# Optimization experiments

Hardware: AMD Instinct MI355X
Metric: run time of the kernel (lower is better)

Reference implementation:

```python
import jax, jax.numpy as jnp
import numpy as np

N_NODES = 50000
N_EDGES = 800000
IN_FEAT = 64
OUT_FEAT = 64
NUM_RELS = 200


def setup_inputs() -> dict:
    key = jax.random.key(0)
    ks = jax.random.split(key, 7)
    feat = jax.random.normal(ks[0], (N_NODES, IN_FEAT), dtype=jnp.float32)
    rel = jax.random.normal(ks[1], (NUM_RELS, IN_FEAT), dtype=jnp.float32)
    # xavier_uniform with relu gain ~ sqrt(2)*sqrt(6/(fan_in+fan_out))
    lim_wn = np.sqrt(2.0) * np.sqrt(6.0 / (4 * IN_FEAT + OUT_FEAT))
    weight_neighbor = jax.random.uniform(ks[2], (4 * IN_FEAT, OUT_FEAT), minval=-lim_wn, maxval=lim_wn, dtype=jnp.float32)
    lim_lw = np.sqrt(2.0) * np.sqrt(6.0 / (IN_FEAT + OUT_FEAT))
    loop_weight = jax.random.uniform(ks[3], (IN_FEAT, OUT_FEAT), minval=-lim_lw, maxval=lim_lw, dtype=jnp.float32)
    src = jax.random.randint(ks[4], (N_EDGES,), 0, N_NODES, dtype=jnp.int32)
    dst = jax.random.randint(ks[5], (N_EDGES,), 0, N_NODES, dtype=jnp.int32)
    etype = jax.random.randint(ks[6], (N_EDGES,), 0, NUM_RELS, dtype=jnp.int32)
    return {"feat": feat, "rel": rel, "weight_neighbor": weight_neighbor,
            "loop_weight": loop_weight, "src": src, "dst": dst, "etype": etype}


def reference(feat, rel, weight_neighbor, loop_weight, src, dst, etype):
    n = feat.shape[0]
    # edge gather
    h = feat[src]            # [E, F]
    r = rel[etype]           # [E, F]
    # message: concat([h+r, h*r, h, r]) @ W  -> [E, out]
    m = jnp.concatenate([h + r, h * r, h, r], axis=1) @ weight_neighbor
    # mean scatter-reduce to destination nodes (zero for isolated nodes, like DGL)
    s = jax.ops.segment_sum(m, dst, num_segments=n)
    cnt = jax.ops.segment_sum(jnp.ones((dst.shape[0],), feat.dtype), dst, num_segments=n)
    agg = s / jnp.maximum(cnt, 1.0)[:, None]
    # self loop (activation=None, dropout=0.0 -> identity)
    return agg + feat @ loop_weight
```

## Files before the change

### kernel.cpp

```cpp
#include <hip/hip_runtime.h>

#define F 64
#define CAP 64
#define CAPB 4608
#define EPB 2048
#define XSTR 264

typedef __attribute__((ext_vector_type(8))) short bf16x8;
typedef __attribute__((ext_vector_type(4))) float f32x4;

__device__ __forceinline__ unsigned short f2b(float x) {
    unsigned int u = __float_as_uint(x);
    return (unsigned short)((u + 0x7FFFu + ((u >> 16) & 1u)) >> 16);
}

__global__ void k_pre(const float* __restrict__ wn, const float* __restrict__ lw,
                      unsigned short* __restrict__ wcb, int* __restrict__ bin_cursor,
                      int nbin) {
    int i = blockIdx.x * 256 + threadIdx.x;
    if (i < nbin) bin_cursor[i] = 0;
    int lane = (i >> 3) & 63, j = i & 7;
    int kt = i >> 11, nt = (i >> 9) & 3;
    int k = kt * 32 + ((lane >> 4) << 3) + j;
    int n = nt * 16 + (lane & 15);
    float v;
    if (k < 64)
        v = wn[k * 64 + n] + wn[(128 + k) * 64 + n];
    else if (k < 128)
        v = wn[(k - 64) * 64 + n] + wn[(k + 128) * 64 + n];
    else if (k < 192)
        v = wn[(k - 64) * 64 + n];
    else
        v = lw[(k - 192) * 64 + n];
    wcb[i] = f2b(v);
}

__global__ __launch_bounds__(256) void k_bin(
    const int* __restrict__ src, const int* __restrict__ dst,
    const int* __restrict__ et, int* __restrict__ bin_cursor,
    unsigned int* __restrict__ coarse, int e) {
    __shared__ int hist[256];
    __shared__ int cur[256];

    const int t = threadIdx.x;
    hist[t] = 0;
    __syncthreads();

    const int i0 = blockIdx.x * EPB + t * 8;
    int s[8], d[8], r[8];
    int nv = 0;
    if (i0 + 8 <= e) {
        int4 sa = ((const int4*)(src + i0))[0], sb = ((const int4*)(src + i0))[1];
        int4 da = ((const int4*)(dst + i0))[0], db = ((const int4*)(dst + i0))[1];
        int4 ta = ((const int4*)(et  + i0))[0], tb = ((const int4*)(et  + i0))[1];
        s[0]=sa.x; s[1]=sa.y; s[2]=sa.z; s[3]=sa.w; s[4]=sb.x; s[5]=sb.y; s[6]=sb.z; s[7]=sb.w;
        d[0]=da.x; d[1]=da.y; d[2]=da.z; d[3]=da.w; d[4]=db.x; d[5]=db.y; d[6]=db.z; d[7]=db.w;
        r[0]=ta.x; r[1]=ta.y; r[2]=ta.z; r[3]=ta.w; r[4]=tb.x; r[5]=tb.y; r[6]=tb.z; r[7]=tb.w;
        nv = 8;
    } else {
        for (int q = 0; q < 8; ++q) {
            int i = i0 + q;
            if (i < e) { s[q] = src[i]; d[q] = dst[i]; r[q] = et[i]; nv = q + 1; }
        }
    }

    for (int q = 0; q < nv; ++q) atomicAdd(&hist[d[q] >> 8], 1);
    __syncthreads();

    if (hist[t] > 0) cur[t] = atomicAdd(&bin_cursor[t], hist[t]);
    __syncthreads();

    for (int q = 0; q < nv; ++q) {
        int b = d[q] >> 8;
        int pos = atomicAdd(&cur[b], 1);
        if (pos < CAPB)
            coarse[b * CAPB + pos] = (unsigned int)s[q] | ((unsigned int)r[q] << 16)
                                   | ((unsigned int)(d[q] & 255) << 24);
    }
}

__global__ __launch_bounds__(1024) void k_build(
    const unsigned int* __restrict__ coarse, const int* __restrict__ bin_cursor,
    unsigned int* __restrict__ bucket, int* __restrict__ cnt, int n) {
    __shared__ int lcnt[256];
    const int t = threadIdx.x, b = blockIdx.x;
    if (t < 256) lcnt[t] = 0;
    __syncthreads();
    int ne = bin_cursor[b]; if (ne > CAPB) ne = CAPB;
    for (int i = t; i < ne; i += 1024) {
        unsigned int u = coarse[b * CAPB + i];
        int dl = (int)(u >> 24);
        int rk = atomicAdd(&lcnt[dl], 1);
        if (rk < CAP) bucket[(((b << 8) | dl) * CAP) + rk] = u & 0xFFFFFFu;
    }
    __syncthreads();
    int node = (b << 8) + t;
    if (t < 256 && node < n) cnt[node] = lcnt[t];
}

#define NPW 4

__global__ __launch_bounds__(256, 8) void k_main(
    const float* __restrict__ feat, const float* __restrict__ rel,
    const unsigned short* __restrict__ wcb, const int* __restrict__ cnt,
    const unsigned int* __restrict__ bucket,
    float* __restrict__ out, int n_nodes) {

    __shared__ unsigned short xb[16 * XSTR];

    const int lane = threadIdx.x & 63;
    const int wid  = threadIdx.x >> 6;
    const int node0 = (blockIdx.x * 4 + wid) * NPW;

#pragma unroll
    for (int n = 0; n < NPW; ++n) {
        int v = node0 + n;
        float sH = 0.f, sR = 0.f, sHR = 0.f, f0 = 0.f;
        if (v < n_nodes) {
            int deg = cnt[v];
            int m = deg < CAP ? deg : CAP;
            unsigned int pk = (lane < m) ? bucket[v * CAP + lane] : 0u;
            int j = 0;
            for (; j + 8 <= m; j += 8) {
                float h[8], r[8];
#pragma unroll
                for (int q = 0; q < 8; ++q) {
                    int u = __builtin_amdgcn_readlane((int)pk, j + q);
                    h[q] = feat[((u & 0xFFFF) << 6) + lane];
                    r[q] = rel[(((u >> 16) & 0xFF) << 6) + lane];
                }
#pragma unroll
                for (int q = 0; q < 8; ++q) {
                    sH += h[q]; sR += r[q]; sHR += h[q] * r[q];
                }
            }
            for (; j < m; ++j) {
                int u = __builtin_amdgcn_readlane((int)pk, j);
                float h = feat[((u & 0xFFFF) << 6) + lane];
                float r = rel[(((u >> 16) & 0xFF) << 6) + lane];
                sH += h; sR += r; sHR += h * r;
            }
            float inv = (deg > 0) ? 1.0f / (float)deg : 1.0f;
            sH *= inv; sR *= inv; sHR *= inv;
            f0 = feat[v * F + lane];
        }
        unsigned short* X = &xb[(wid * NPW + n) * XSTR];
        X[lane]       = f2b(sH);
        X[64 + lane]  = f2b(sR);
        X[128 + lane] = f2b(sHR);
        X[192 + lane] = f2b(f0);
    }
    __syncthreads();

    f32x4 acc = {0.f, 0.f, 0.f, 0.f};
    const int am = lane & 15, aq = lane >> 4;
#pragma unroll
    for (int kt = 0; kt < 8; ++kt) {
        bf16x8 a = *(const bf16x8*)&xb[am * XSTR + kt * 32 + aq * 8];
        bf16x8 b = *(const bf16x8*)&wcb[(((kt * 4 + wid) * 64) + lane) * 8];
        acc = __builtin_amdgcn_mfma_f32_16x16x32_bf16(a, b, acc, 0, 0, 0);
    }

    const int colbase = wid * 16 + am;
#pragma unroll
    for (int reg = 0; reg < 4; ++reg) {
        int v = blockIdx.x * 16 + aq * 4 + reg;
        if (v < n_nodes) out[v * F + colbase] = acc[reg];
    }
}

extern "C" void kernel_launch(void* const* d_in, const int* in_sizes, int n_in,
                              void* d_out, int out_size, void* d_ws, size_t ws_size,
                              hipStream_t stream) {
    const float* feat = (const float*)d_in[0];
    const float* rel  = (const float*)d_in[1];
    const float* wn   = (const float*)d_in[2];
    const float* lw   = (const float*)d_in[3];
    const int* src = (const int*)d_in[4];
    const int* dst = (const int*)d_in[5];
    const int* et  = (const int*)d_in[6];
    float* out = (float*)d_out;

    const int N = in_sizes[0] / F;
    const int E = in_sizes[4];
    const int nbin = (N + 255) >> 8;

    int* ws = (int*)d_ws;
    int* bin_cursor      = ws;
    int* cnt             = ws + 256;
    unsigned int* coarse = (unsigned int*)(cnt + N);
    unsigned int* bucket = coarse + (size_t)nbin * CAPB;
    unsigned short* wcb  = (unsigned short*)(bucket + (size_t)N * CAP);

    k_pre<<<64, 256, 0, stream>>>(wn, lw, wcb, bin_cursor, nbin);
    k_bin<<<(E + EPB - 1) / EPB, 256, 0, stream>>>(src, dst, et, bin_cursor, coarse, E);
    k_build<<<nbin, 1024, 0, stream>>>(coarse, bin_cursor, bucket, cnt, N);
    int blocks = (N + 15) / 16;
    k_main<<<blocks, 256, 0, stream>>>(feat, rel, wcb, cnt, bucket, out, N);
}
```

Before: 137.6 us.

## Gather two edges per wave with float2 half-wave loads; enlarge binning blocks

The main gather loop now has each half-wave fetch a different edge's 64-float row as float2 loads, so one wave instruction covers two edges. The two halves' partial sums are combined with a cross-half shuffle before the bf16 packing, and the LDS stores become packed 32-bit writes split between halves. Separately, the binning kernel processes twice as many edges per block with 512 threads, which halves the number of blocks and global cursor atomics. The aim is fewer load instructions and more bytes per load in the gather, at the cost of extra shuffles and select logic for odd-degree tails.

```diff
diff --git a/kernel.cpp b/kernel.cpp
--- a/kernel.cpp
+++ b/kernel.cpp
@@ -3,7 +3,7 @@
 #define F 64
 #define CAP 64
 #define CAPB 4608
-#define EPB 2048
+#define EPB 4096
 #define XSTR 264
 
 typedef __attribute__((ext_vector_type(8))) short bf16x8;
@@ -35,7 +35,7 @@
     wcb[i] = f2b(v);
 }
 
-__global__ __launch_bounds__(256) void k_bin(
+__global__ __launch_bounds__(512) void k_bin(
     const int* __restrict__ src, const int* __restrict__ dst,
     const int* __restrict__ et, int* __restrict__ bin_cursor,
     unsigned int* __restrict__ coarse, int e) {
@@ -43,7 +43,7 @@
     __shared__ int cur[256];
 
     const int t = threadIdx.x;
-    hist[t] = 0;
+    if (t < 256) hist[t] = 0;
     __syncthreads();
 
     const int i0 = blockIdx.x * EPB + t * 8;
@@ -67,7 +67,7 @@
     for (int q = 0; q < nv; ++q) atomicAdd(&hist[d[q] >> 8], 1);
     __syncthreads();
 
-    if (hist[t] > 0) cur[t] = atomicAdd(&bin_cursor[t], hist[t]);
+    if (t < 256 && hist[t] > 0) cur[t] = atomicAdd(&bin_cursor[t], hist[t]);
     __syncthreads();
 
     for (int q = 0; q < nv; ++q) {
@@ -110,45 +110,74 @@
 
     const int lane = threadIdx.x & 63;
     const int wid  = threadIdx.x >> 6;
+    const int lf   = lane & 31;
+    const bool hi  = lane >= 32;
+    const float zm = hi ? 0.f : 1.f;
     const int node0 = (blockIdx.x * 4 + wid) * NPW;
+
+    const float2* f2 = (const float2*)feat;
+    const float2* r2 = (const float2*)rel;
 
 #pragma unroll
     for (int n = 0; n < NPW; ++n) {
         int v = node0 + n;
-        float sH = 0.f, sR = 0.f, sHR = 0.f, f0 = 0.f;
+        float2 sH = {0.f, 0.f}, sR = {0.f, 0.f}, sHR = {0.f, 0.f}, f02 = {0.f, 0.f};
         if (v < n_nodes) {
             int deg = cnt[v];
             int m = deg < CAP ? deg : CAP;
             unsigned int pk = (lane < m) ? bucket[v * CAP + lane] : 0u;
             int j = 0;
             for (; j + 8 <= m; j += 8) {
-                float h[8], r[8];
-#pragma unroll
-                for (int q = 0; q < 8; ++q) {
-                    int u = __builtin_amdgcn_readlane((int)pk, j + q);
-                    h[q] = feat[((u & 0xFFFF) << 6) + lane];
-                    r[q] = rel[(((u >> 16) & 0xFF) << 6) + lane];
+                float2 h[4], r[4];
+#pragma unroll
+                for (int p = 0; p < 4; ++p) {
+                    int u0 = __builtin_amdgcn_readlane((int)pk, j + 2 * p);
+                    int u1 = __builtin_amdgcn_readlane((int)pk, j + 2 * p + 1);
+                    int u = hi ? u1 : u0;
+                    h[p] = f2[((u & 0xFFFF) << 5) + lf];
+                    r[p] = r2[(((u >> 16) & 0xFF) << 5) + lf];
                 }
 #pragma unroll
-                for (int q = 0; q < 8; ++q) {
-                    sH += h[q]; sR += r[q]; sHR += h[q] * r[q];
+                for (int p = 0; p < 4; ++p) {
+                    sH.x += h[p].x;            sH.y += h[p].y;
+                    sR.x += r[p].x;            sR.y += r[p].y;
+                    sHR.x += h[p].x * r[p].x;  sHR.y += h[p].y * r[p].y;
                 }
             }
-            for (; j < m; ++j) {
+            for (; j + 2 <= m; j += 2) {
+                int u0 = __builtin_amdgcn_readlane((int)pk, j);
+                int u1 = __builtin_amdgcn_readlane((int)pk, j + 1);
+                int u = hi ? u1 : u0;
+                float2 h = f2[((u & 0xFFFF) << 5) + lf];
+                float2 r = r2[(((u >> 16) & 0xFF) << 5) + lf];
+                sH.x += h.x;          sH.y += h.y;
+                sR.x += r.x;          sR.y += r.y;
+                sHR.x += h.x * r.x;   sHR.y += h.y * r.y;
+            }
+            if (j < m) {
                 int u = __builtin_amdgcn_readlane((int)pk, j);
-                float h = feat[((u & 0xFFFF) << 6) + lane];
-                float r = rel[(((u >> 16) & 0xFF) << 6) + lane];
-                sH += h; sR += r; sHR += h * r;
+                float2 h = f2[((u & 0xFFFF) << 5) + lf];
+                float2 r = r2[(((u >> 16) & 0xFF) << 5) + lf];
+                h.x *= zm; h.y *= zm; r.x *= zm; r.y *= zm;
+                sH.x += h.x;          sH.y += h.y;
+                sR.x += r.x;          sR.y += r.y;
+                sHR.x += h.x * r.x;   sHR.y += h.y * r.y;
             }
+            sH.x += __shfl_xor(sH.x, 32);   sH.y += __shfl_xor(sH.y, 32);
+            sR.x += __shfl_xor(sR.x, 32);   sR.y += __shfl_xor(sR.y, 32);
+            sHR.x += __shfl_xor(sHR.x, 32); sHR.y += __shfl_xor(sHR.y, 32);
             float inv = (deg > 0) ? 1.0f / (float)deg : 1.0f;
-            sH *= inv; sR *= inv; sHR *= inv;
-            f0 = feat[v * F + lane];
+            sH.x *= inv; sH.y *= inv; sR.x *= inv; sR.y *= inv;
+            sHR.x *= inv; sHR.y *= inv;
+            f02 = f2[(v << 5) + lf];
         }
-        unsigned short* X = &xb[(wid * NPW + n) * XSTR];
-        X[lane]       = f2b(sH);
-        X[64 + lane]  = f2b(sR);
-        X[128 + lane] = f2b(sHR);
-        X[192 + lane] = f2b(f0);
+        unsigned int pH = ((unsigned int)f2b(sH.y) << 16) | f2b(sH.x);
+        unsigned int pR = ((unsigned int)f2b(sR.y) << 16) | f2b(sR.x);
+        unsigned int pQ = ((unsigned int)f2b(sHR.y) << 16) | f2b(sHR.x);
+        unsigned int pF = ((unsigned int)f2b(f02.y) << 16) | f2b(f02.x);
+        unsigned int* X32 = (unsigned int*)&xb[(wid * NPW + n) * XSTR];
+        if (!hi) { X32[lf] = pH;      X32[64 + lf] = pQ; }
+        else     { X32[32 + lf] = pR; X32[96 + lf] = pF; }
     }
     __syncthreads();
 
@@ -193,7 +222,7 @@
     unsigned short* wcb  = (unsigned short*)(bucket + (size_t)N * CAP);
 
     k_pre<<<64, 256, 0, stream>>>(wn, lw, wcb, bin_cursor, nbin);
-    k_bin<<<(E + EPB - 1) / EPB, 256, 0, stream>>>(src, dst, et, bin_cursor, coarse, E);
+    k_bin<<<(E + EPB - 1) / EPB, 512, 0, stream>>>(src, dst, et, bin_cursor, coarse, E);
     k_build<<<nbin, 1024, 0, stream>>>(coarse, bin_cursor, bucket, cnt, N);
     int blocks = (N + 15) / 16;
     k_main<<<blocks, 256, 0, stream>>>(feat, rel, wcb, cnt, bucket, out, N);
```

Result: no change. 135.2 us (-1.7%).

## Interleave two nodes' edge gathers per wave and widen binning blocks

Applied to the files above, without the earlier changes.

The main kernel now processes node pairs, issuing the 8-edge feature and relation gathers for both nodes before accumulating either. This puts more independent global loads in flight per wave to hide gather latency. The binning kernel moves to 1024-thread blocks handling 8192 edges each, which cuts global cursor atomics but launches far fewer blocks. Mean normalization now divides by the capped degree instead of the true degree, which only matters for nodes with more than 64 edges.

```diff
diff --git a/kernel.cpp b/kernel.cpp
--- a/kernel.cpp
+++ b/kernel.cpp
@@ -3,7 +3,7 @@
 #define F 64
 #define CAP 64
 #define CAPB 4608
-#define EPB 2048
+#define EPB 8192
 #define XSTR 264
 
 typedef __attribute__((ext_vector_type(8))) short bf16x8;
@@ -35,7 +35,7 @@
     wcb[i] = f2b(v);
 }
 
-__global__ __launch_bounds__(256) void k_bin(
+__global__ __launch_bounds__(1024) void k_bin(
     const int* __restrict__ src, const int* __restrict__ dst,
     const int* __restrict__ et, int* __restrict__ bin_cursor,
     unsigned int* __restrict__ coarse, int e) {
@@ -43,7 +43,7 @@
     __shared__ int cur[256];
 
     const int t = threadIdx.x;
-    hist[t] = 0;
+    if (t < 256) hist[t] = 0;
     __syncthreads();
 
     const int i0 = blockIdx.x * EPB + t * 8;
@@ -67,7 +67,7 @@
     for (int q = 0; q < nv; ++q) atomicAdd(&hist[d[q] >> 8], 1);
     __syncthreads();
 
-    if (hist[t] > 0) cur[t] = atomicAdd(&bin_cursor[t], hist[t]);
+    if (t < 256 && hist[t] > 0) cur[t] = atomicAdd(&bin_cursor[t], hist[t]);
     __syncthreads();
 
     for (int q = 0; q < nv; ++q) {
@@ -113,42 +113,78 @@
     const int node0 = (blockIdx.x * 4 + wid) * NPW;
 
 #pragma unroll
-    for (int n = 0; n < NPW; ++n) {
-        int v = node0 + n;
-        float sH = 0.f, sR = 0.f, sHR = 0.f, f0 = 0.f;
-        if (v < n_nodes) {
-            int deg = cnt[v];
-            int m = deg < CAP ? deg : CAP;
-            unsigned int pk = (lane < m) ? bucket[v * CAP + lane] : 0u;
-            int j = 0;
-            for (; j + 8 <= m; j += 8) {
-                float h[8], r[8];
-#pragma unroll
-                for (int q = 0; q < 8; ++q) {
-                    int u = __builtin_amdgcn_readlane((int)pk, j + q);
-                    h[q] = feat[((u & 0xFFFF) << 6) + lane];
-                    r[q] = rel[(((u >> 16) & 0xFF) << 6) + lane];
-                }
-#pragma unroll
-                for (int q = 0; q < 8; ++q) {
-                    sH += h[q]; sR += r[q]; sHR += h[q] * r[q];
-                }
-            }
-            for (; j < m; ++j) {
-                int u = __builtin_amdgcn_readlane((int)pk, j);
-                float h = feat[((u & 0xFFFF) << 6) + lane];
-                float r = rel[(((u >> 16) & 0xFF) << 6) + lane];
-                sH += h; sR += r; sHR += h * r;
-            }
-            float inv = (deg > 0) ? 1.0f / (float)deg : 1.0f;
-            sH *= inv; sR *= inv; sHR *= inv;
-            f0 = feat[v * F + lane];
-        }
-        unsigned short* X = &xb[(wid * NPW + n) * XSTR];
-        X[lane]       = f2b(sH);
-        X[64 + lane]  = f2b(sR);
-        X[128 + lane] = f2b(sHR);
-        X[192 + lane] = f2b(f0);
+    for (int np = 0; np < NPW; np += 2) {
+        const int va = node0 + np, vb = node0 + np + 1;
+        const int ma = (va < n_nodes) ? min(cnt[va], CAP) : 0;
+        const int mb = (vb < n_nodes) ? min(cnt[vb], CAP) : 0;
+        unsigned int pka = (lane < ma) ? bucket[va * CAP + lane] : 0u;
+        unsigned int pkb = (lane < mb) ? bucket[vb * CAP + lane] : 0u;
+        float sHa = 0.f, sRa = 0.f, sQa = 0.f;
+        float sHb = 0.f, sRb = 0.f, sQb = 0.f;
+        int ja = 0, jb = 0;
+
+        while ((ja + 8 <= ma) | (jb + 8 <= mb)) {
+            const bool da = (ja + 8 <= ma), db = (jb + 8 <= mb);
+            float ha[8], ra[8], hb[8], rb[8];
+            if (da) {
+#pragma unroll
+                for (int q = 0; q < 8; ++q) {
+                    int u = __builtin_amdgcn_readlane((int)pka, ja + q);
+                    ha[q] = feat[((u & 0xFFFF) << 6) + lane];
+                    ra[q] = rel[(((u >> 16) & 0xFF) << 6) + lane];
+                }
+            }
+            if (db) {
+#pragma unroll
+                for (int q = 0; q < 8; ++q) {
+                    int u = __builtin_amdgcn_readlane((int)pkb, jb + q);
+                    hb[q] = feat[((u & 0xFFFF) << 6) + lane];
+                    rb[q] = rel[(((u >> 16) & 0xFF) << 6) + lane];
+                }
+            }
+            if (da) {
+#pragma unroll
+                for (int q = 0; q < 8; ++q) {
+                    sHa += ha[q]; sRa += ra[q]; sQa += ha[q] * ra[q];
+                }
+                ja += 8;
+            }
+            if (db) {
+#pragma unroll
+                for (int q = 0; q < 8; ++q) {
+                    sHb += hb[q]; sRb += rb[q]; sQb += hb[q] * rb[q];
+                }
+                jb += 8;
+            }
+        }
+        for (; ja < ma; ++ja) {
+            int u = __builtin_amdgcn_readlane((int)pka, ja);
+            float h = feat[((u & 0xFFFF) << 6) + lane];
+            float r = rel[(((u >> 16) & 0xFF) << 6) + lane];
+            sHa += h; sRa += r; sQa += h * r;
+        }
+        for (; jb < mb; ++jb) {
+            int u = __builtin_amdgcn_readlane((int)pkb, jb);
+            float h = feat[((u & 0xFFFF) << 6) + lane];
+            float r = rel[(((u >> 16) & 0xFF) << 6) + lane];
+            sHb += h; sRb += r; sQb += h * r;
+        }
+
+        const float inva = (ma > 0) ? 1.0f / (float)ma : 1.0f;
+        const float invb = (mb > 0) ? 1.0f / (float)mb : 1.0f;
+        const float f0a = (va < n_nodes) ? feat[va * F + lane] : 0.f;
+        const float f0b = (vb < n_nodes) ? feat[vb * F + lane] : 0.f;
+
+        unsigned short* Xa = &xb[(wid * NPW + np) * XSTR];
+        Xa[lane]       = f2b(sHa * inva);
+        Xa[64 + lane]  = f2b(sRa * inva);
+        Xa[128 + lane] = f2b(sQa * inva);
+        Xa[192 + lane] = f2b(f0a);
+        unsigned short* Xb = &xb[(wid * NPW + np + 1) * XSTR];
+        Xb[lane]       = f2b(sHb * invb);
+        Xb[64 + lane]  = f2b(sRb * invb);
+        Xb[128 + lane] = f2b(sQb * invb);
+        Xb[192 + lane] = f2b(f0b);
     }
     __syncthreads();
 
@@ -193,7 +229,7 @@
     unsigned short* wcb  = (unsigned short*)(bucket + (size_t)N * CAP);
 
     k_pre<<<64, 256, 0, stream>>>(wn, lw, wcb, bin_cursor, nbin);
-    k_bin<<<(E + EPB - 1) / EPB, 256, 0, stream>>>(src, dst, et, bin_cursor, coarse, E);
+    k_bin<<<(E + EPB - 1) / EPB, 1024, 0, stream>>>(src, dst, et, bin_cursor, coarse, E);
     k_build<<<nbin, 1024, 0, stream>>>(coarse, bin_cursor, bucket, cnt, N);
     int blocks = (N + 15) / 16;
     k_main<<<blocks, 256, 0, stream>>>(feat, rel, wcb, cnt, bucket, out, N);
```

Result: no change. 135.1 us (-1.8%).

## Pre-convert feat and rel to bf16 for gathers; enlarge binning blocks

Applied to the files above, without the earlier changes.

Adds a conversion pass in the prologue kernel that writes bf16 copies of feat and rel, and the main kernel gathers from those copies, halving the bytes moved per random edge gather. The binning kernel also moves to 1024-thread blocks handling 8192 edges each, which cuts the number of blocks and the global cursor atomics. The conversion adds a full read and write of feat, and summing bf16-rounded inputs adds precision loss beyond the existing bf16 MFMA stage.

```diff
diff --git a/kernel.cpp b/kernel.cpp
--- a/kernel.cpp
+++ b/kernel.cpp
@@ -3,7 +3,7 @@
 #define F 64
 #define CAP 64
 #define CAPB 4608
-#define EPB 2048
+#define EPB 8192
 #define XSTR 264
 
 typedef __attribute__((ext_vector_type(8))) short bf16x8;
@@ -13,29 +13,50 @@
     unsigned int u = __float_as_uint(x);
     return (unsigned short)((u + 0x7FFFu + ((u >> 16) & 1u)) >> 16);
 }
+__device__ __forceinline__ float b2f(unsigned short b) {
+    return __uint_as_float(((unsigned int)b) << 16);
+}
 
 __global__ void k_pre(const float* __restrict__ wn, const float* __restrict__ lw,
-                      unsigned short* __restrict__ wcb, int* __restrict__ bin_cursor,
-                      int nbin) {
-    int i = blockIdx.x * 256 + threadIdx.x;
-    if (i < nbin) bin_cursor[i] = 0;
-    int lane = (i >> 3) & 63, j = i & 7;
-    int kt = i >> 11, nt = (i >> 9) & 3;
-    int k = kt * 32 + ((lane >> 4) << 3) + j;
-    int n = nt * 16 + (lane & 15);
-    float v;
-    if (k < 64)
-        v = wn[k * 64 + n] + wn[(128 + k) * 64 + n];
-    else if (k < 128)
-        v = wn[(k - 64) * 64 + n] + wn[(k + 128) * 64 + n];
-    else if (k < 192)
-        v = wn[(k - 64) * 64 + n];
-    else
-        v = lw[(k - 192) * 64 + n];
-    wcb[i] = f2b(v);
-}
-
-__global__ __launch_bounds__(256) void k_bin(
+                      const float* __restrict__ feat, const float* __restrict__ rel,
+                      unsigned short* __restrict__ wcb, unsigned short* __restrict__ fb,
+                      unsigned short* __restrict__ rb, int* __restrict__ bin_cursor,
+                      int nbin, int nf4, int nr4) {
+    if (blockIdx.x < 64) {
+        int i = blockIdx.x * 256 + threadIdx.x;
+        if (i < nbin) bin_cursor[i] = 0;
+        int lane = (i >> 3) & 63, j = i & 7;
+        int kt = i >> 11, nt = (i >> 9) & 3;
+        int k = kt * 32 + ((lane >> 4) << 3) + j;
+        int n = nt * 16 + (lane & 15);
+        float v;
+        if (k < 64)
+            v = wn[k * 64 + n] + wn[(128 + k) * 64 + n];
+        else if (k < 128)
+            v = wn[(k - 64) * 64 + n] + wn[(k + 128) * 64 + n];
+        else if (k < 192)
+            v = wn[(k - 64) * 64 + n];
+        else
+            v = lw[(k - 192) * 64 + n];
+        wcb[i] = f2b(v);
+        return;
+    }
+    int c = (blockIdx.x - 64) * 256 + threadIdx.x;
+    if (c < nf4) {
+        float4 q = ((const float4*)feat)[c];
+        ushort4 o;
+        o.x = f2b(q.x); o.y = f2b(q.y); o.z = f2b(q.z); o.w = f2b(q.w);
+        ((ushort4*)fb)[c] = o;
+    } else if (c - nf4 < nr4) {
+        int j = c - nf4;
+        float4 q = ((const float4*)rel)[j];
+        ushort4 o;
+        o.x = f2b(q.x); o.y = f2b(q.y); o.z = f2b(q.z); o.w = f2b(q.w);
+        ((ushort4*)rb)[j] = o;
+    }
+}
+
+__global__ __launch_bounds__(1024) void k_bin(
     const int* __restrict__ src, const int* __restrict__ dst,
     const int* __restrict__ et, int* __restrict__ bin_cursor,
     unsigned int* __restrict__ coarse, int e) {
@@ -43,7 +64,7 @@
     __shared__ int cur[256];
 
     const int t = threadIdx.x;
-    hist[t] = 0;
+    if (t < 256) hist[t] = 0;
     __syncthreads();
 
     const int i0 = blockIdx.x * EPB + t * 8;
@@ -67,7 +88,7 @@
     for (int q = 0; q < nv; ++q) atomicAdd(&hist[d[q] >> 8], 1);
     __syncthreads();
 
-    if (hist[t] > 0) cur[t] = atomicAdd(&bin_cursor[t], hist[t]);
+    if (t < 256 && hist[t] > 0) cur[t] = atomicAdd(&bin_cursor[t], hist[t]);
     __syncthreads();
 
     for (int q = 0; q < nv; ++q) {
@@ -101,7 +122,7 @@
 #define NPW 4
 
 __global__ __launch_bounds__(256, 8) void k_main(
-    const float* __restrict__ feat, const float* __restrict__ rel,
+    const unsigned short* __restrict__ fb, const unsigned short* __restrict__ rb,
     const unsigned short* __restrict__ wcb, const int* __restrict__ cnt,
     const unsigned int* __restrict__ bucket,
     float* __restrict__ out, int n_nodes) {
@@ -126,8 +147,8 @@
 #pragma unroll
                 for (int q = 0; q < 8; ++q) {
                     int u = __builtin_amdgcn_readlane((int)pk, j + q);
-                    h[q] = feat[((u & 0xFFFF) << 6) + lane];
-                    r[q] = rel[(((u >> 16) & 0xFF) << 6) + lane];
+                    h[q] = b2f(fb[((u & 0xFFFF) << 6) + lane]);
+                    r[q] = b2f(rb[(((u >> 16) & 0xFF) << 6) + lane]);
                 }
 #pragma unroll
                 for (int q = 0; q < 8; ++q) {
@@ -136,13 +157,13 @@
             }
             for (; j < m; ++j) {
                 int u = __builtin_amdgcn_readlane((int)pk, j);
-                float h = feat[((u & 0xFFFF) << 6) + lane];
-                float r = rel[(((u >> 16) & 0xFF) << 6) + lane];
+                float h = b2f(fb[((u & 0xFFFF) << 6) + lane]);
+                float r = b2f(rb[(((u >> 16) & 0xFF) << 6) + lane]);
                 sH += h; sR += r; sHR += h * r;
             }
             float inv = (deg > 0) ? 1.0f / (float)deg : 1.0f;
             sH *= inv; sR *= inv; sHR *= inv;
-            f0 = feat[v * F + lane];
+            f0 = b2f(fb[v * F + lane]);
         }
         unsigned short* X = &xb[(wid * NPW + n) * XSTR];
         X[lane]       = f2b(sH);
@@ -182,8 +203,10 @@
     float* out = (float*)d_out;
 
     const int N = in_sizes[0] / F;
+    const int R = in_sizes[1] / F;
     const int E = in_sizes[4];
     const int nbin = (N + 255) >> 8;
+    const int NF4 = N * F / 4, NR4 = R * F / 4;
 
     int* ws = (int*)d_ws;
     int* bin_cursor      = ws;
@@ -191,10 +214,14 @@
     unsigned int* coarse = (unsigned int*)(cnt + N);
     unsigned int* bucket = coarse + (size_t)nbin * CAPB;
     unsigned short* wcb  = (unsigned short*)(bucket + (size_t)N * CAP);
-
-    k_pre<<<64, 256, 0, stream>>>(wn, lw, wcb, bin_cursor, nbin);
-    k_bin<<<(E + EPB - 1) / EPB, 256, 0, stream>>>(src, dst, et, bin_cursor, coarse, E);
+    unsigned short* fb   = wcb + 16384;
+    unsigned short* rb   = fb + (size_t)N * F;
+
+    int conv_blocks = (NF4 + NR4 + 255) / 256;
+    k_pre<<<64 + conv_blocks, 256, 0, stream>>>(wn, lw, feat, rel, wcb, fb, rb,
+                                                bin_cursor, nbin, NF4, NR4);
+    k_bin<<<(E + EPB - 1) / EPB, 1024, 0, stream>>>(src, dst, et, bin_cursor, coarse, E);
     k_build<<<nbin, 1024, 0, stream>>>(coarse, bin_cursor, bucket, cnt, N);
     int blocks = (N + 15) / 16;
-    k_main<<<blocks, 256, 0, stream>>>(feat, rel, wcb, cnt, bucket, out, N);
-}
+    k_main<<<blocks, 256, 0, stream>>>(fb, rb, wcb, cnt, bucket, out, N);
+}
```

Result: faster. 133.6 us (-2.9%).
